# Performance work log

Measured on AMD Instinct MI355X. Metric: run time of the kernel, lower is better.

## Reference

```python
import jax, jax.numpy as jnp
import numpy as np
from jax import lax

B, T, D, L, H = 512, 512, 64, 32, 128


def setup_inputs() -> dict:
    key = jax.random.key(0)
    ks = jax.random.split(key, 18)
    s = 0.08  # keep recurrent dynamics stable
    return {
        "x": jax.random.normal(ks[0], (B, T, D), dtype=jnp.float32),
        "eps": jax.random.normal(ks[1], (B, L), dtype=jnp.float32),
        "enc_W_ih": jax.random.normal(ks[2], (4 * H, D), dtype=jnp.float32) * s,
        "enc_W_hh": jax.random.normal(ks[3], (4 * H, H), dtype=jnp.float32) * s,
        "enc_b_ih": jax.random.normal(ks[4], (4 * H,), dtype=jnp.float32) * s,
        "enc_b_hh": jax.random.normal(ks[5], (4 * H,), dtype=jnp.float32) * s,
        "mu_W": jax.random.normal(ks[6], (L, H), dtype=jnp.float32) * s,
        "mu_b": jax.random.normal(ks[7], (L,), dtype=jnp.float32) * s,
        "lv_W": jax.random.normal(ks[8], (L, H), dtype=jnp.float32) * s,
        "lv_b": jax.random.normal(ks[9], (L,), dtype=jnp.float32) * s,
        "init_W": jax.random.normal(ks[10], (H, L), dtype=jnp.float32) * s,
        "init_b": jax.random.normal(ks[11], (H,), dtype=jnp.float32) * s,
        "dec_W_ih": jax.random.normal(ks[12], (4 * H, D), dtype=jnp.float32) * s,
        "dec_W_hh": jax.random.normal(ks[13], (4 * H, H), dtype=jnp.float32) * s,
        "dec_b_ih": jax.random.normal(ks[14], (4 * H,), dtype=jnp.float32) * s,
        "dec_b_hh": jax.random.normal(ks[15], (4 * H,), dtype=jnp.float32) * s,
        "out_W": jax.random.normal(ks[16], (D, H), dtype=jnp.float32) * s,
        "out_b": jax.random.normal(ks[17], (D,), dtype=jnp.float32) * s,
    }


def _lstm_update(gates, c):
    # PyTorch gate order: input, forget, cell(g), output
    i, f, g, o = jnp.split(gates, 4, axis=-1)
    c_new = jax.nn.sigmoid(f) * c + jax.nn.sigmoid(i) * jnp.tanh(g)
    h_new = jax.nn.sigmoid(o) * jnp.tanh(c_new)
    return h_new, c_new


def reference(x, eps, enc_W_ih, enc_W_hh, enc_b_ih, enc_b_hh,
              mu_W, mu_b, lv_W, lv_b, init_W, init_b,
              dec_W_ih, dec_W_hh, dec_b_ih, dec_b_hh, out_W, out_b):
    Bn, Tn, Dn = x.shape
    Hn = enc_W_hh.shape[1]

    # ---- encoder LSTM (batch_first) ----
    # precompute input projections for all timesteps: [T, B, 4H]
    gx = (jnp.einsum('btd,gd->btg', x, enc_W_ih) + enc_b_ih + enc_b_hh)
    gx = gx.transpose(1, 0, 2)

    def enc_step(carry, g):
        h, c = carry
        gates = g + h @ enc_W_hh.T
        h, c = _lstm_update(gates, c)
        return (h, c), None

    h0 = jnp.zeros((Bn, Hn), x.dtype)
    (hT, _), _ = lax.scan(enc_step, (h0, h0), gx)

    mu = hT @ mu_W.T + mu_b
    log_var = hT @ lv_W.T + lv_b
    z = mu + eps * jnp.exp(0.5 * log_var)  # reparameterize

    h_dec = z @ init_W.T + init_b  # decoder_hidden_init (no activation)
    c_dec = jnp.zeros_like(h_dec)
    inp0 = jnp.zeros((Bn, Dn), x.dtype)
    bd = dec_b_ih + dec_b_hh

    def dec_step(carry, _):
        h, c, inp = carry
        gates = inp @ dec_W_ih.T + h @ dec_W_hh.T + bd
        h, c = _lstm_update(gates, c)
        y = h @ out_W.T + out_b  # fc_decode_output; also next input
        return (h, c, y), y

    _, ys = lax.scan(dec_step, (h_dec, c_dec, inp0), None, length=Tn)
    x_rec = ys.transpose(1, 0, 2)  # [B, T, D]
    return x_rec, mu, log_var
```

## Files before the change

### kernel.cpp

```cpp
#include <hip/hip_runtime.h>

#define Bn 512
#define Tn 512
#define Dn 64
#define Hn 128
#define Ln 32

typedef __attribute__((ext_vector_type(8))) short short8v;
typedef __attribute__((ext_vector_type(4))) float float4v;

__device__ __forceinline__ unsigned short f2bf(float f){
  unsigned int u = __float_as_uint(f);
  u += 0x7FFFu + ((u >> 16) & 1u);
  return (unsigned short)(u >> 16);
}

__device__ __forceinline__ short8v pack8(float4v a, float4v b){
  short8v r;
  r[0]=(short)f2bf(a[0]); r[1]=(short)f2bf(a[1]);
  r[2]=(short)f2bf(a[2]); r[3]=(short)f2bf(a[3]);
  r[4]=(short)f2bf(b[0]); r[5]=(short)f2bf(b[1]);
  r[6]=(short)f2bf(b[2]); r[7]=(short)f2bf(b[3]);
  return r;
}

__device__ __forceinline__ unsigned long long pack4u64(float4v v){
  return (unsigned long long)f2bf(v[0])
       | ((unsigned long long)f2bf(v[1])<<16)
       | ((unsigned long long)f2bf(v[2])<<32)
       | ((unsigned long long)f2bf(v[3])<<48);
}

__device__ __forceinline__ short8v load_wfrag(const float* __restrict__ W, int n, int k0, int ldk){
  const float* p = W + (size_t)n*(size_t)ldk + (size_t)k0;
  float4v a = *(const float4v*)p;
  float4v b = *(const float4v*)(p+4);
  return pack8(a,b);
}

__device__ __forceinline__ float4v mfma16(short8v a, short8v b, float4v c){
  return __builtin_amdgcn_mfma_f32_16x16x32_bf16(a, b, c, 0, 0, 0);
}

__device__ __forceinline__ float sigm(float v){
  return __builtin_amdgcn_rcpf(1.0f + __expf(-v));
}
__device__ __forceinline__ float tanh_(float v){
  return 1.0f - 2.0f*__builtin_amdgcn_rcpf(1.0f + __expf(2.0f*v));
}

__device__ __forceinline__ void bar_lds(){
  __builtin_amdgcn_sched_barrier(0);
  asm volatile("s_waitcnt lgkmcnt(0)" ::: "memory");
  __builtin_amdgcn_s_barrier();
  __builtin_amdgcn_sched_barrier(0);
}

__global__ __launch_bounds__(256) void weff_kernel(
    const float* __restrict__ dW_ih, const float* __restrict__ dW_hh,
    const float* __restrict__ db_ih, const float* __restrict__ db_hh,
    const float* __restrict__ oW,    const float* __restrict__ ob,
    float* __restrict__ ws)
{
  int id = blockIdx.x*256 + threadIdx.x;
  if (id < 512*128) {
    int n = id >> 7, h = id & 127;
    float s = dW_hh[id];
    #pragma unroll 8
    for (int d = 0; d < Dn; ++d) s += dW_ih[n*Dn + d] * oW[d*Hn + h];
    ws[id] = s;
  } else if (id < 512*128 + 512) {
    int n = id - 512*128;
    float s = db_ih[n] + db_hh[n];
    #pragma unroll 8
    for (int d = 0; d < Dn; ++d) s += dW_ih[n*Dn + d] * ob[d];
    ws[512*128 + n] = s;
  }
}

__global__ __launch_bounds__(256, 1) void vae_fused(
    const float* __restrict__ x,     const float* __restrict__ eps,
    const float* __restrict__ eW_ih, const float* __restrict__ eW_hh,
    const float* __restrict__ eb_ih, const float* __restrict__ eb_hh,
    const float* __restrict__ muW,   const float* __restrict__ mub,
    const float* __restrict__ lvW,   const float* __restrict__ lvb,
    const float* __restrict__ iW,    const float* __restrict__ ib,
    const float* __restrict__ dW_hh, const float* __restrict__ db_ih,
    const float* __restrict__ db_hh, const float* __restrict__ oW,
    const float* __restrict__ ob,    const float* __restrict__ ws,
    float* __restrict__ out)
{
  __shared__ __align__(16) unsigned short x_s[2*Tn*Dn];
  __shared__ __align__(16) unsigned short h_lds[2*2*128];
  __shared__ __align__(16) float sc_h[2*Hn];
  __shared__ __align__(16) float sc_mu[2*Ln];
  __shared__ __align__(16) float sc_lv[2*Ln];
  __shared__ __align__(16) float sc_z[2*Ln];

  const int tid  = threadIdx.x;
  const int lane = tid & 63;
  const int w    = tid >> 6;
  const int m    = lane & 15;
  const int q    = lane >> 4;
  const int hrow = m & 1;
  const int half_= q & 1;
  const int r_   = q >> 1;
  const int jown = w*32 + half_*16 + m;
  const int b0   = blockIdx.x * 2;
  char* const hw_p  = (char*)h_lds + r_*256 + ((2*jown) ^ (r_<<4));
  const char* const hr_p = (const char*)h_lds + hrow*256 + ((q*16) ^ (hrow<<4));
  const char* const xr_p = (const char*)x_s + hrow*65536 + q*16;

  {
    const float* xr = x + (size_t)b0 * Tn * Dn;
    #pragma unroll 4
    for (int k2 = 0; k2 < 64; ++k2) {
      int idx4 = tid + k2*256;
      float4v v = *(const float4v*)(xr + (size_t)idx4*4);
      *(unsigned long long*)((char*)x_s + (size_t)idx4*8) = pack4u64(v);
    }
  }
  ((int*)h_lds)[tid] = 0;

  short8v wih[16];
  short8v whh[32];
  #pragma unroll
  for (int nt = 0; nt < 8; ++nt) {
    const int n = (nt>>1)*128 + w*32 + (nt&1)*16 + m;
    #pragma unroll
    for (int kt = 0; kt < 2; ++kt) wih[nt*2+kt] = load_wfrag(eW_ih, n, kt*32 + q*8, Dn);
    #pragma unroll
    for (int kt = 0; kt < 4; ++kt) whh[nt*4+kt] = load_wfrag(eW_hh, n, kt*32 + q*8, Hn);
  }
  float bia[4];
  #pragma unroll
  for (int g = 0; g < 4; ++g) bia[g] = eb_ih[g*128 + jown] + eb_hh[g*128 + jown];

  float cst = 0.0f, hval = 0.0f;
  __syncthreads();

#define READ_HFRAG(RB, KB) (*(const short8v*)(hr_p + (RB)*512 + (KB)))
#define READ_XFRAG(T, KT)  (*(const short8v*)(xr_p + (T)*128 + (KT)*64))

#define NONLIN_WRITE(ACC, WB) do { \
    float gi = half_ ? (r_ ? (ACC)[1][1] : (ACC)[1][0]) : (r_ ? (ACC)[0][1] : (ACC)[0][0]); \
    float gf = half_ ? (r_ ? (ACC)[3][1] : (ACC)[3][0]) : (r_ ? (ACC)[2][1] : (ACC)[2][0]); \
    float gg = half_ ? (r_ ? (ACC)[5][1] : (ACC)[5][0]) : (r_ ? (ACC)[4][1] : (ACC)[4][0]); \
    float go = half_ ? (r_ ? (ACC)[7][1] : (ACC)[7][0]) : (r_ ? (ACC)[6][1] : (ACC)[6][0]); \
    gi += bia[0]; gf += bia[1]; gg += bia[2]; go += bia[3]; \
    float c  = sigm(gf)*cst + sigm(gi)*tanh_(gg); \
    cst = c; \
    hval = sigm(go)*tanh_(c); \
    *(unsigned short*)(hw_p + (WB)*512) = f2bf(hval); \
  } while(0)

#define KSLOT(AF, KI) \
    _Pragma("unroll") \
    for (int nt = 0; nt < 8; ++nt) acc[nt] = mfma16((AF), whh[nt*4+(KI)], acc[nt]);

#define ENC_STEP(T, RB) do { \
    short8v hf0 = READ_HFRAG(RB,0),  hf1 = READ_HFRAG(RB,64); \
    short8v hf2 = READ_HFRAG(RB,128), hf3 = READ_HFRAG(RB,192); \
    short8v xf0 = READ_XFRAG(T,0), xf1 = READ_XFRAG(T,1); \
    float4v acc[8]; \
    _Pragma("unroll") \
    for (int nt = 0; nt < 8; ++nt) { \
      float4v z = {0.f,0.f,0.f,0.f}; \
      acc[nt] = mfma16(xf0, wih[nt*2+0], z); \
    } \
    _Pragma("unroll") \
    for (int nt = 0; nt < 8; ++nt) acc[nt] = mfma16(xf1, wih[nt*2+1], acc[nt]); \
    KSLOT(hf0, 0) KSLOT(hf1, 1) KSLOT(hf2, 2) KSLOT(hf3, 3) \
    NONLIN_WRITE(acc, (RB)^1); \
    __syncthreads(); \
  } while(0)

  for (int t = 0; t < Tn; t += 2) {
    ENC_STEP(t,   0);
    ENC_STEP(t+1, 1);
  }

  sc_h[r_*Hn + jown] = hval;
  __syncthreads();

  if (tid < 128) {
    const int isLv = tid >> 6;
    const int rr   = (tid >> 5) & 1;
    const int l    = tid & 31;
    const float* Wp = isLv ? lvW : muW;
    float s = isLv ? lvb[l] : mub[l];
    #pragma unroll
    for (int k = 0; k < Hn; k += 4) {
      float4v wv = *(const float4v*)(Wp + l*Hn + k);
      float4v hv = *(const float4v*)(sc_h + rr*Hn + k);
      s += wv[0]*hv[0] + wv[1]*hv[1] + wv[2]*hv[2] + wv[3]*hv[3];
    }
    out[(size_t)Bn*Tn*Dn + (size_t)isLv*Bn*Ln + (size_t)(b0+rr)*Ln + l] = s;
    (isLv ? sc_lv : sc_mu)[rr*Ln + l] = s;
  }
  __syncthreads();

  if (tid < 64) {
    int rr = tid >> 5, l = tid & 31;
    sc_z[rr*Ln+l] = sc_mu[rr*Ln+l] + eps[(size_t)(b0+rr)*Ln + l] * __expf(0.5f * sc_lv[rr*Ln+l]);
  }
  __syncthreads();

  {
    int rr = tid >> 7, jj = tid & 127;
    float s = ib[jj];
    #pragma unroll
    for (int l = 0; l < Ln; ++l) s += sc_z[rr*Ln + l] * iW[jj*Ln + l];
    *(unsigned short*)((char*)h_lds + rr*256 + ((2*jj) ^ (rr<<4))) = f2bf(s);
  }
  cst = 0.0f;

  #pragma unroll
  for (int nt = 0; nt < 8; ++nt) {
    const int n = (nt>>1)*128 + w*32 + (nt&1)*16 + m;
    #pragma unroll
    for (int kt = 0; kt < 4; ++kt) whh[nt*4+kt] = load_wfrag(dW_hh, n, kt*32 + q*8, Hn);
  }
  #pragma unroll
  for (int g = 0; g < 4; ++g) bia[g] = db_ih[g*128 + jown] + db_hh[g*128 + jown];
  short8v ow0 = load_wfrag(oW, w*16+m,  0 + q*8, Hn);
  short8v ow1 = load_wfrag(oW, w*16+m, 32 + q*8, Hn);
  short8v ow2 = load_wfrag(oW, w*16+m, 64 + q*8, Hn);
  short8v ow3 = load_wfrag(oW, w*16+m, 96 + q*8, Hn);
  const float obv = ob[w*16+m];
  __syncthreads();

  {
    short8v hf0 = READ_HFRAG(0,0),  hf1 = READ_HFRAG(0,64);
    short8v hf2 = READ_HFRAG(0,128), hf3 = READ_HFRAG(0,192);
    float4v acc[8];
    #pragma unroll
    for (int nt = 0; nt < 8; ++nt) {
      float4v z = {0.f,0.f,0.f,0.f};
      acc[nt] = mfma16(hf0, whh[nt*4+0], z);
    }
    KSLOT(hf1, 1) KSLOT(hf2, 2) KSLOT(hf3, 3)
    NONLIN_WRITE(acc, 1);
    __syncthreads();
  }

  {
    const float* weff = ws;
    const float* beff = ws + 512*128;
    #pragma unroll
    for (int nt = 0; nt < 8; ++nt) {
      const int n = (nt>>1)*128 + w*32 + (nt&1)*16 + m;
      #pragma unroll
      for (int kt = 0; kt < 4; ++kt) whh[nt*4+kt] = load_wfrag(weff, n, kt*32 + q*8, Hn);
    }
    #pragma unroll
    for (int g = 0; g < 4; ++g) bia[g] = beff[g*128 + jown];
  }

  float* outp0 = out + (size_t)(b0+0)*Tn*Dn;
  float* outp1 = out + (size_t)(b0+1)*Tn*Dn;
  const int ocol = w*16 + lane;

#define DEC_STEP(RB) do { \
    short8v hf0 = READ_HFRAG(RB,0),  hf1 = READ_HFRAG(RB,64); \
    short8v hf2 = READ_HFRAG(RB,128), hf3 = READ_HFRAG(RB,192); \
    float4v acc[8]; float4v ya; \
    { float4v z = {0.f,0.f,0.f,0.f}; \
      _Pragma("unroll") \
      for (int nt = 0; nt < 8; ++nt) acc[nt] = mfma16(hf0, whh[nt*4+0], z); \
      ya = mfma16(hf0, ow0, z); } \
    KSLOT(hf1, 1) ya = mfma16(hf1, ow1, ya); \
    KSLOT(hf2, 2) ya = mfma16(hf2, ow2, ya); \
    KSLOT(hf3, 3) ya = mfma16(hf3, ow3, ya); \
    if (lane < 16) { \
      outp0[ocol] = ya[0] + obv; \
      outp1[ocol] = ya[1] + obv; \
    } \
    outp0 += Dn; outp1 += Dn; \
    NONLIN_WRITE(acc, (RB)^1); \
    bar_lds(); \
  } while(0)

  for (int i = 1; i < Tn-1; i += 2) {
    DEC_STEP(1);
    DEC_STEP(0);
  }
  DEC_STEP(1);

  {
    short8v hf0 = READ_HFRAG(0,0),  hf1 = READ_HFRAG(0,64);
    short8v hf2 = READ_HFRAG(0,128), hf3 = READ_HFRAG(0,192);
    float4v ya = {0.f,0.f,0.f,0.f};
    ya = mfma16(hf0, ow0, ya); ya = mfma16(hf1, ow1, ya);
    ya = mfma16(hf2, ow2, ya); ya = mfma16(hf3, ow3, ya);
    if (lane < 16) {
      outp0[ocol] = ya[0] + obv;
      outp1[ocol] = ya[1] + obv;
    }
  }
#undef DEC_STEP
#undef ENC_STEP
#undef KSLOT
#undef NONLIN_WRITE
#undef READ_HFRAG
#undef READ_XFRAG
}

extern "C" void kernel_launch(void* const* d_in, const int* in_sizes, int n_in,
                              void* d_out, int out_size, void* d_ws, size_t ws_size,
                              hipStream_t stream) {
  (void)in_sizes; (void)n_in; (void)ws_size; (void)out_size;
  const float* x     = (const float*)d_in[0];
  const float* eps   = (const float*)d_in[1];
  const float* eW_ih = (const float*)d_in[2];
  const float* eW_hh = (const float*)d_in[3];
  const float* eb_ih = (const float*)d_in[4];
  const float* eb_hh = (const float*)d_in[5];
  const float* muW   = (const float*)d_in[6];
  const float* mub   = (const float*)d_in[7];
  const float* lvW   = (const float*)d_in[8];
  const float* lvb   = (const float*)d_in[9];
  const float* iW    = (const float*)d_in[10];
  const float* ib    = (const float*)d_in[11];
  const float* dW_ih = (const float*)d_in[12];
  const float* dW_hh = (const float*)d_in[13];
  const float* db_ih = (const float*)d_in[14];
  const float* db_hh = (const float*)d_in[15];
  const float* oW    = (const float*)d_in[16];
  const float* ob    = (const float*)d_in[17];
  float* out = (float*)d_out;
  float* ws  = (float*)d_ws;

  weff_kernel<<<dim3(258), dim3(256), 0, stream>>>(dW_ih, dW_hh, db_ih, db_hh, oW, ob, ws);
  vae_fused<<<dim3(256), dim3(256), 0, stream>>>(
      x, eps, eW_ih, eW_hh, eb_ih, eb_hh, muW, mub, lvW, lvb,
      iW, ib, dW_hh, db_ih, db_hh, oW, ob, ws, out);
}
```

Measured before the change: 609.6 us.

## Split LSTM gates over 8 waves and batch encoder input projections per 8 steps

After: 696.8 us. 14.3% more time.

```diff
diff --git a/kernel.cpp b/kernel.cpp
--- a/kernel.cpp
+++ b/kernel.cpp
@@ -8,6 +8,7 @@
 
 typedef __attribute__((ext_vector_type(8))) short short8v;
 typedef __attribute__((ext_vector_type(4))) float float4v;
+typedef __attribute__((ext_vector_type(2))) float float2v;
 
 __device__ __forceinline__ unsigned short f2bf(float f){
   unsigned int u = __float_as_uint(f);
@@ -22,13 +23,6 @@
   r[4]=(short)f2bf(b[0]); r[5]=(short)f2bf(b[1]);
   r[6]=(short)f2bf(b[2]); r[7]=(short)f2bf(b[3]);
   return r;
-}
-
-__device__ __forceinline__ unsigned long long pack4u64(float4v v){
-  return (unsigned long long)f2bf(v[0])
-       | ((unsigned long long)f2bf(v[1])<<16)
-       | ((unsigned long long)f2bf(v[2])<<32)
-       | ((unsigned long long)f2bf(v[3])<<48);
 }
 
 __device__ __forceinline__ short8v load_wfrag(const float* __restrict__ W, int n, int k0, int ldk){
@@ -78,7 +72,7 @@
   }
 }
 
-__global__ __launch_bounds__(256, 1) void vae_fused(
+__global__ __launch_bounds__(512, 2) void vae_fused(
     const float* __restrict__ x,     const float* __restrict__ eps,
     const float* __restrict__ eW_ih, const float* __restrict__ eW_hh,
     const float* __restrict__ eb_ih, const float* __restrict__ eb_hh,
@@ -90,7 +84,7 @@
     const float* __restrict__ ob,    const float* __restrict__ ws,
     float* __restrict__ out)
 {
-  __shared__ __align__(16) unsigned short x_s[2*Tn*Dn];
+  __shared__ __align__(16) float gxb[8*4*128*2];
   __shared__ __align__(16) unsigned short h_lds[2*2*128];
   __shared__ __align__(16) float sc_h[2*Hn];
   __shared__ __align__(16) float sc_mu[2*Ln];
@@ -103,84 +97,106 @@
   const int m    = lane & 15;
   const int q    = lane >> 4;
   const int hrow = m & 1;
-  const int half_= q & 1;
-  const int r_   = q >> 1;
-  const int jown = w*32 + half_*16 + m;
+  const int jown = w*16 + m;
   const int b0   = blockIdx.x * 2;
-  char* const hw_p  = (char*)h_lds + r_*256 + ((2*jown) ^ (r_<<4));
+  char* const hwq_p = (char*)h_lds + q*256 + ((2*jown) ^ (q<<4));
   const char* const hr_p = (const char*)h_lds + hrow*256 + ((q*16) ^ (hrow<<4));
-  const char* const xr_p = (const char*)x_s + hrow*65536 + q*16;
-
-  {
-    const float* xr = x + (size_t)b0 * Tn * Dn;
-    #pragma unroll 4
-    for (int k2 = 0; k2 < 64; ++k2) {
-      int idx4 = tid + k2*256;
-      float4v v = *(const float4v*)(xr + (size_t)idx4*4);
-      *(unsigned long long*)((char*)x_s + (size_t)idx4*8) = pack4u64(v);
-    }
-  }
-  ((int*)h_lds)[tid] = 0;
-
-  short8v wih[16];
-  short8v whh[32];
+  const char* const gx_p = (const char*)gxb + jown*8;
+  char* const gw_p = (char*)gxb + jown*8 + q*8192;
+
+  if (tid < 256) ((int*)h_lds)[tid] = 0;
+
+  short8v wih[8];
+  short8v whh[16];
   #pragma unroll
-  for (int nt = 0; nt < 8; ++nt) {
-    const int n = (nt>>1)*128 + w*32 + (nt&1)*16 + m;
-    #pragma unroll
-    for (int kt = 0; kt < 2; ++kt) wih[nt*2+kt] = load_wfrag(eW_ih, n, kt*32 + q*8, Dn);
-    #pragma unroll
-    for (int kt = 0; kt < 4; ++kt) whh[nt*4+kt] = load_wfrag(eW_hh, n, kt*32 + q*8, Hn);
+  for (int nt = 0; nt < 4; ++nt) {
+    #pragma unroll
+    for (int kt = 0; kt < 2; ++kt) wih[nt*2+kt] = load_wfrag(eW_ih, nt*128 + jown, kt*32 + q*8, Dn);
+    #pragma unroll
+    for (int kt = 0; kt < 4; ++kt) whh[nt*4+kt] = load_wfrag(eW_hh, nt*128 + jown, kt*32 + q*8, Hn);
   }
   float bia[4];
   #pragma unroll
   for (int g = 0; g < 4; ++g) bia[g] = eb_ih[g*128 + jown] + eb_hh[g*128 + jown];
 
-  float cst = 0.0f, hval = 0.0f;
-  __syncthreads();
-
-#define READ_HFRAG(RB, KB) (*(const short8v*)(hr_p + (RB)*512 + (KB)))
-#define READ_XFRAG(T, KT)  (*(const short8v*)(xr_p + (T)*128 + (KT)*64))
-
-#define NONLIN_WRITE(ACC, WB) do { \
-    float gi = half_ ? (r_ ? (ACC)[1][1] : (ACC)[1][0]) : (r_ ? (ACC)[0][1] : (ACC)[0][0]); \
-    float gf = half_ ? (r_ ? (ACC)[3][1] : (ACC)[3][0]) : (r_ ? (ACC)[2][1] : (ACC)[2][0]); \
-    float gg = half_ ? (r_ ? (ACC)[5][1] : (ACC)[5][0]) : (r_ ? (ACC)[4][1] : (ACC)[4][0]); \
-    float go = half_ ? (r_ ? (ACC)[7][1] : (ACC)[7][0]) : (r_ ? (ACC)[6][1] : (ACC)[6][0]); \
-    gi += bia[0]; gf += bia[1]; gg += bia[2]; go += bia[3]; \
-    float c  = sigm(gf)*cst + sigm(gi)*tanh_(gg); \
-    cst = c; \
-    hval = sigm(go)*tanh_(c); \
-    *(unsigned short*)(hw_p + (WB)*512) = f2bf(hval); \
+  const float* xbase = x + (size_t)(b0 + hrow)*Tn*Dn + (size_t)(m>>1)*Dn + q*8;
+  float4v xc0,xc1,xc2,xc3, xn0,xn1,xn2,xn3;
+  xc0 = *(const float4v*)(xbase+0);  xc1 = *(const float4v*)(xbase+4);
+  xc2 = *(const float4v*)(xbase+32); xc3 = *(const float4v*)(xbase+36);
+
+  float cst0 = 0.f, cst1 = 0.f, h0 = 0.f, h1 = 0.f;
+  __syncthreads();
+
+#define RH(RB,KB)  (*(const short8v*)(hr_p + (RB)*512 + (KB)))
+#define RGX(S,NT)  (*(const float2v*)(gx_p + (S)*4096 + (NT)*1024))
+
+#define BATCH(TB) do { \
+    short8v xf0 = pack8(xc0, xc1); \
+    short8v xf1 = pack8(xc2, xc3); \
+    if ((TB) < 63) { \
+      const float* xp = xbase + ((TB)+1)*512; \
+      xn0 = *(const float4v*)(xp+0);  xn1 = *(const float4v*)(xp+4); \
+      xn2 = *(const float4v*)(xp+32); xn3 = *(const float4v*)(xp+36); \
+    } \
+    float4v zz = {0.f,0.f,0.f,0.f}; \
+    float4v c0_ = mfma16(xf0, wih[0], zz); \
+    float4v c1_ = mfma16(xf0, wih[2], zz); \
+    float4v c2_ = mfma16(xf0, wih[4], zz); \
+    float4v c3_ = mfma16(xf0, wih[6], zz); \
+    c0_ = mfma16(xf1, wih[1], c0_); \
+    c1_ = mfma16(xf1, wih[3], c1_); \
+    c2_ = mfma16(xf1, wih[5], c2_); \
+    c3_ = mfma16(xf1, wih[7], c3_); \
+    *(float2v*)(gw_p +        0) = (float2v){c0_[0]+bia[0], c0_[1]+bia[0]}; \
+    *(float2v*)(gw_p +     1024) = (float2v){c1_[0]+bia[1], c1_[1]+bia[1]}; \
+    *(float2v*)(gw_p +     2048) = (float2v){c2_[0]+bia[2], c2_[1]+bia[2]}; \
+    *(float2v*)(gw_p +     3072) = (float2v){c3_[0]+bia[3], c3_[1]+bia[3]}; \
+    *(float2v*)(gw_p + 4096 + 0)    = (float2v){c0_[2]+bia[0], c0_[3]+bia[0]}; \
+    *(float2v*)(gw_p + 4096 + 1024) = (float2v){c1_[2]+bia[1], c1_[3]+bia[1]}; \
+    *(float2v*)(gw_p + 4096 + 2048) = (float2v){c2_[2]+bia[2], c2_[3]+bia[2]}; \
+    *(float2v*)(gw_p + 4096 + 3072) = (float2v){c3_[2]+bia[3], c3_[3]+bia[3]}; \
+    xc0=xn0; xc1=xn1; xc2=xn2; xc3=xn3; \
+    bar_lds(); \
   } while(0)
 
-#define KSLOT(AF, KI) \
-    _Pragma("unroll") \
-    for (int nt = 0; nt < 8; ++nt) acc[nt] = mfma16((AF), whh[nt*4+(KI)], acc[nt]);
-
-#define ENC_STEP(T, RB) do { \
-    short8v hf0 = READ_HFRAG(RB,0),  hf1 = READ_HFRAG(RB,64); \
-    short8v hf2 = READ_HFRAG(RB,128), hf3 = READ_HFRAG(RB,192); \
-    short8v xf0 = READ_XFRAG(T,0), xf1 = READ_XFRAG(T,1); \
-    float4v acc[8]; \
-    _Pragma("unroll") \
-    for (int nt = 0; nt < 8; ++nt) { \
-      float4v z = {0.f,0.f,0.f,0.f}; \
-      acc[nt] = mfma16(xf0, wih[nt*2+0], z); \
-    } \
-    _Pragma("unroll") \
-    for (int nt = 0; nt < 8; ++nt) acc[nt] = mfma16(xf1, wih[nt*2+1], acc[nt]); \
-    KSLOT(hf0, 0) KSLOT(hf1, 1) KSLOT(hf2, 2) KSLOT(hf3, 3) \
-    NONLIN_WRITE(acc, (RB)^1); \
-    __syncthreads(); \
+#define NONLIN2(GI0,GI1,GF0,GF1,GG0,GG1,GO0,GO1, WB) do { \
+    float nc0 = sigm(GF0)*cst0 + sigm(GI0)*tanh_(GG0); \
+    float nc1 = sigm(GF1)*cst1 + sigm(GI1)*tanh_(GG1); \
+    cst0 = nc0; cst1 = nc1; \
+    h0 = sigm(GO0)*tanh_(nc0); h1 = sigm(GO1)*tanh_(nc1); \
+    if (q < 2) *(unsigned short*)(hwq_p + (WB)*512) = f2bf(q ? h1 : h0); \
   } while(0)
 
-  for (int t = 0; t < Tn; t += 2) {
-    ENC_STEP(t,   0);
-    ENC_STEP(t+1, 1);
-  }
-
-  sc_h[r_*Hn + jown] = hval;
+#define HH16(RB) \
+    short8v hf0 = RH(RB,0), hf1 = RH(RB,64), hf2 = RH(RB,128), hf3 = RH(RB,192); \
+    float4v zz = {0.f,0.f,0.f,0.f}; \
+    float4v a0 = mfma16(hf0, whh[0],  zz); \
+    float4v a1 = mfma16(hf0, whh[4],  zz); \
+    float4v a2 = mfma16(hf0, whh[8],  zz); \
+    float4v a3 = mfma16(hf0, whh[12], zz); \
+    a0 = mfma16(hf1, whh[1],  a0); a1 = mfma16(hf1, whh[5],  a1); \
+    a2 = mfma16(hf1, whh[9],  a2); a3 = mfma16(hf1, whh[13], a3); \
+    a0 = mfma16(hf2, whh[2],  a0); a1 = mfma16(hf2, whh[6],  a1); \
+    a2 = mfma16(hf2, whh[10], a2); a3 = mfma16(hf2, whh[14], a3); \
+    a0 = mfma16(hf3, whh[3],  a0); a1 = mfma16(hf3, whh[7],  a1); \
+    a2 = mfma16(hf3, whh[11], a2); a3 = mfma16(hf3, whh[15], a3);
+
+#define ENC_STEP(S, RB) do { \
+    float2v g0 = RGX(S,0), g1 = RGX(S,1), g2 = RGX(S,2), g3 = RGX(S,3); \
+    HH16(RB); \
+    NONLIN2(a0[0]+g0[0], a0[1]+g0[1], a1[0]+g1[0], a1[1]+g1[1], \
+            a2[0]+g2[0], a2[1]+g2[1], a3[0]+g3[0], a3[1]+g3[1], (RB)^1); \
+    bar_lds(); \
+  } while(0)
+
+  #pragma unroll 1
+  for (int tb = 0; tb < 64; ++tb) {
+    BATCH(tb);
+    ENC_STEP(0,0); ENC_STEP(1,1); ENC_STEP(2,0); ENC_STEP(3,1);
+    ENC_STEP(4,0); ENC_STEP(5,1); ENC_STEP(6,0); ENC_STEP(7,1);
+  }
+
+  if (q == 0) { sc_h[jown] = h0; sc_h[Hn + jown] = h1; }
   __syncthreads();
 
   if (tid < 128) {
@@ -206,104 +222,87 @@
   }
   __syncthreads();
 
-  {
+  if (tid < 256) {
     int rr = tid >> 7, jj = tid & 127;
     float s = ib[jj];
     #pragma unroll
     for (int l = 0; l < Ln; ++l) s += sc_z[rr*Ln + l] * iW[jj*Ln + l];
     *(unsigned short*)((char*)h_lds + rr*256 + ((2*jj) ^ (rr<<4))) = f2bf(s);
   }
-  cst = 0.0f;
+  cst0 = 0.f; cst1 = 0.f;
 
   #pragma unroll
-  for (int nt = 0; nt < 8; ++nt) {
-    const int n = (nt>>1)*128 + w*32 + (nt&1)*16 + m;
-    #pragma unroll
-    for (int kt = 0; kt < 4; ++kt) whh[nt*4+kt] = load_wfrag(dW_hh, n, kt*32 + q*8, Hn);
-  }
+  for (int nt = 0; nt < 4; ++nt)
+    #pragma unroll
+    for (int kt = 0; kt < 4; ++kt) whh[nt*4+kt] = load_wfrag(dW_hh, nt*128 + jown, kt*32 + q*8, Hn);
   #pragma unroll
   for (int g = 0; g < 4; ++g) bia[g] = db_ih[g*128 + jown] + db_hh[g*128 + jown];
-  short8v ow0 = load_wfrag(oW, w*16+m,  0 + q*8, Hn);
-  short8v ow1 = load_wfrag(oW, w*16+m, 32 + q*8, Hn);
-  short8v ow2 = load_wfrag(oW, w*16+m, 64 + q*8, Hn);
-  short8v ow3 = load_wfrag(oW, w*16+m, 96 + q*8, Hn);
-  const float obv = ob[w*16+m];
+  const int ocol = (w & 3)*16 + m;
+  short8v ow0 = load_wfrag(oW, ocol,  0 + q*8, Hn);
+  short8v ow1 = load_wfrag(oW, ocol, 32 + q*8, Hn);
+  short8v ow2 = load_wfrag(oW, ocol, 64 + q*8, Hn);
+  short8v ow3 = load_wfrag(oW, ocol, 96 + q*8, Hn);
+  const float obv = ob[ocol];
   __syncthreads();
 
   {
-    short8v hf0 = READ_HFRAG(0,0),  hf1 = READ_HFRAG(0,64);
-    short8v hf2 = READ_HFRAG(0,128), hf3 = READ_HFRAG(0,192);
-    float4v acc[8];
-    #pragma unroll
-    for (int nt = 0; nt < 8; ++nt) {
-      float4v z = {0.f,0.f,0.f,0.f};
-      acc[nt] = mfma16(hf0, whh[nt*4+0], z);
-    }
-    KSLOT(hf1, 1) KSLOT(hf2, 2) KSLOT(hf3, 3)
-    NONLIN_WRITE(acc, 1);
-    __syncthreads();
+    HH16(0);
+    NONLIN2(a0[0]+bia[0], a0[1]+bia[0], a1[0]+bia[1], a1[1]+bia[1],
+            a2[0]+bia[2], a2[1]+bia[2], a3[0]+bia[3], a3[1]+bia[3], 1);
+    bar_lds();
   }
 
   {
     const float* weff = ws;
     const float* beff = ws + 512*128;
     #pragma unroll
-    for (int nt = 0; nt < 8; ++nt) {
-      const int n = (nt>>1)*128 + w*32 + (nt&1)*16 + m;
+    for (int nt = 0; nt < 4; ++nt)
       #pragma unroll
-      for (int kt = 0; kt < 4; ++kt) whh[nt*4+kt] = load_wfrag(weff, n, kt*32 + q*8, Hn);
-    }
+      for (int kt = 0; kt < 4; ++kt) whh[nt*4+kt] = load_wfrag(weff, nt*128 + jown, kt*32 + q*8, Hn);
     #pragma unroll
     for (int g = 0; g < 4; ++g) bia[g] = beff[g*128 + jown];
   }
 
   float* outp0 = out + (size_t)(b0+0)*Tn*Dn;
   float* outp1 = out + (size_t)(b0+1)*Tn*Dn;
-  const int ocol = w*16 + lane;
 
 #define DEC_STEP(RB) do { \
-    short8v hf0 = READ_HFRAG(RB,0),  hf1 = READ_HFRAG(RB,64); \
-    short8v hf2 = READ_HFRAG(RB,128), hf3 = READ_HFRAG(RB,192); \
-    float4v acc[8]; float4v ya; \
-    { float4v z = {0.f,0.f,0.f,0.f}; \
-      _Pragma("unroll") \
-      for (int nt = 0; nt < 8; ++nt) acc[nt] = mfma16(hf0, whh[nt*4+0], z); \
-      ya = mfma16(hf0, ow0, z); } \
-    KSLOT(hf1, 1) ya = mfma16(hf1, ow1, ya); \
-    KSLOT(hf2, 2) ya = mfma16(hf2, ow2, ya); \
-    KSLOT(hf3, 3) ya = mfma16(hf3, ow3, ya); \
-    if (lane < 16) { \
-      outp0[ocol] = ya[0] + obv; \
-      outp1[ocol] = ya[1] + obv; \
+    HH16(RB); \
+    if (w < 4) { \
+      float4v ya = mfma16(hf0, ow0, zz); \
+      ya = mfma16(hf1, ow1, ya); ya = mfma16(hf2, ow2, ya); ya = mfma16(hf3, ow3, ya); \
+      if (q == 0) { outp0[ocol] = ya[0] + obv; outp1[ocol] = ya[1] + obv; } \
     } \
     outp0 += Dn; outp1 += Dn; \
-    NONLIN_WRITE(acc, (RB)^1); \
+    NONLIN2(a0[0]+bia[0], a0[1]+bia[0], a1[0]+bia[1], a1[1]+bia[1], \
+            a2[0]+bia[2], a2[1]+bia[2], a3[0]+bia[3], a3[1]+bia[3], (RB)^1); \
     bar_lds(); \
   } while(0)
 
+  #pragma unroll 1
   for (int i = 1; i < Tn-1; i += 2) {
     DEC_STEP(1);
     DEC_STEP(0);
   }
   DEC_STEP(1);
 
-  {
-    short8v hf0 = READ_HFRAG(0,0),  hf1 = READ_HFRAG(0,64);
-    short8v hf2 = READ_HFRAG(0,128), hf3 = READ_HFRAG(0,192);
+  if (w < 4) {
+    short8v hf0 = RH(0,0), hf1 = RH(0,64), hf2 = RH(0,128), hf3 = RH(0,192);
     float4v ya = {0.f,0.f,0.f,0.f};
     ya = mfma16(hf0, ow0, ya); ya = mfma16(hf1, ow1, ya);
     ya = mfma16(hf2, ow2, ya); ya = mfma16(hf3, ow3, ya);
-    if (lane < 16) {
+    if (q == 0) {
       outp0[ocol] = ya[0] + obv;
       outp1[ocol] = ya[1] + obv;
     }
   }
 #undef DEC_STEP
 #undef ENC_STEP
-#undef KSLOT
-#undef NONLIN_WRITE
-#undef READ_HFRAG
-#undef READ_XFRAG
+#undef HH16
+#undef NONLIN2
+#undef BATCH
+#undef RGX
+#undef RH
 }
 
 extern "C" void kernel_launch(void* const* d_in, const int* in_sizes, int n_in,
@@ -332,7 +331,7 @@
   float* ws  = (float*)d_ws;
 
   weff_kernel<<<dim3(258), dim3(256), 0, stream>>>(dW_ih, dW_hh, db_ih, db_hh, oW, ob, ws);
-  vae_fused<<<dim3(256), dim3(256), 0, stream>>>(
+  vae_fused<<<dim3(256), dim3(512), 0, stream>>>(
       x, eps, eW_ih, eW_hh, eb_ih, eb_hh, muW, mub, lvW, lvb,
       iW, ib, dW_hh, db_ih, db_hh, oW, ob, ws, out);
 }
```
